# Kernel optimization log

Hardware: AMD Instinct MI355X
Metric: run time of the kernel (lower is better)

## Reference

```python
import jax, jax.numpy as jnp
import numpy as np

OUT_FEATURES = 4096
IN_FEATURES = 4096

# NF4 codebook (bitsandbytes normal-float 4-bit values)
_NF4_CODEBOOK = np.array([
    -1.0, -0.6961928, -0.52507305, -0.3949175, -0.28444138, -0.18477343,
    -0.09105004, 0.0, 0.0795803, 0.1609302, 0.2461123, 0.33791524,
    0.44070983, 0.562617, 0.72295684, 1.0], dtype=np.float32)


def setup_inputs() -> dict:
    key = jax.random.key(0)
    k_x, k_codes, k_scale, k_bias = jax.random.split(key, 4)
    x = jax.random.normal(k_x, (4, 2048, IN_FEATURES), dtype=jnp.float32)
    # packed uint8 nibble codes stored as int32 in [0, 256)
    packed_codes = jax.random.randint(
        k_codes, (OUT_FEATURES * IN_FEATURES // 2,), 0, 256, dtype=jnp.int32)
    # positive per-channel scales [out, 1]
    scale = jax.random.uniform(k_scale, (OUT_FEATURES, 1), dtype=jnp.float32) * 0.05 + 0.01
    bias = jax.random.normal(k_bias, (OUT_FEATURES,), dtype=jnp.float32)
    return {"x": x, "packed_codes": packed_codes, "scale": scale, "bias": bias}


def _dequantize_nf4(packed_codes, scale):
    codebook = jnp.asarray(_NF4_CODEBOOK)
    low = packed_codes & 15           # even positions
    high = (packed_codes >> 4) & 15   # odd positions
    # interleave: unpacked[0::2]=low, unpacked[1::2]=high
    idx = jnp.stack([low, high], axis=-1).reshape(-1)  # [out*in]
    w = codebook[idx].reshape(OUT_FEATURES, IN_FEATURES) * scale  # [out, in]
    return w


def reference(x, packed_codes, scale, bias):
    w = _dequantize_nf4(packed_codes, scale)
    # F.linear: x @ w.T + bias
    return jnp.einsum("bsi,oi->bso", x, w) + bias
```

## Files before the change

kernel.cpp:

```cpp
#include <hip/hip_runtime.h>
#include <stdint.h>

#define IN_F 4096
#define OUT_F 4096
#define M_ROWS 8192

__device__ __constant__ int c_nf4_i8[16] = {
    -127, -88, -67, -50, -36, -23, -12, 0, 10, 20, 31, 43, 56, 71, 92, 127};

typedef int i32x4 __attribute__((ext_vector_type(4)));

__global__ __launch_bounds__(256) void k_quant_x(
    const float* __restrict__ x, signed char* __restrict__ xq,
    float* __restrict__ steps) {
  const int row = blockIdx.x;
  const int tid = threadIdx.x;
  const float4* xr = (const float4*)(x + (size_t)row * IN_F);
  float4 v[4];
  float m = 0.0f;
#pragma unroll
  for (int i = 0; i < 4; ++i) {
    v[i] = xr[tid + 256 * i];
    m = fmaxf(m, fmaxf(fmaxf(fabsf(v[i].x), fabsf(v[i].y)),
                       fmaxf(fabsf(v[i].z), fabsf(v[i].w))));
  }
#pragma unroll
  for (int off = 32; off > 0; off >>= 1) m = fmaxf(m, __shfl_xor(m, off));
  __shared__ float wmax[4];
  if ((tid & 63) == 0) wmax[tid >> 6] = m;
  __syncthreads();
  m = fmaxf(fmaxf(wmax[0], wmax[1]), fmaxf(wmax[2], wmax[3]));
  const float inv = (m > 0.0f) ? 127.0f / m : 0.0f;
  if (tid == 0) steps[row] = m * (1.0f / 127.0f);
  int* oq = (int*)(xq + (size_t)row * IN_F);
#pragma unroll
  for (int i = 0; i < 4; ++i) {
    int q0 = (int)rintf(v[i].x * inv);
    int q1 = (int)rintf(v[i].y * inv);
    int q2 = (int)rintf(v[i].z * inv);
    int q3 = (int)rintf(v[i].w * inv);
    oq[tid + 256 * i] =
        (q0 & 255) | ((q1 & 255) << 8) | ((q2 & 255) << 16) | (q3 << 24);
  }
}

__global__ __launch_bounds__(256) void k_dequant(
    const int* __restrict__ packed, signed char* __restrict__ W) {
  __shared__ short lut[256];
  {
    const int b = threadIdx.x;
    const int lo = c_nf4_i8[b & 15], hi = c_nf4_i8[b >> 4];
    lut[b] = (short)((lo & 0xFF) | ((hi & 0xFF) << 8));
  }
  __syncthreads();
  const int tid = blockIdx.x * 256 + threadIdx.x;
  const int4 ca = ((const int4*)packed)[2 * tid];
  const int4 cb = ((const int4*)packed)[2 * tid + 1];
  union { short h[8]; int4 v; } o;
  o.h[0] = lut[ca.x]; o.h[1] = lut[ca.y]; o.h[2] = lut[ca.z]; o.h[3] = lut[ca.w];
  o.h[4] = lut[cb.x]; o.h[5] = lut[cb.y]; o.h[6] = lut[cb.z]; o.h[7] = lut[cb.w];
  ((int4*)W)[tid] = o.v;
}

#define GLL(gptr, lptr)                                          \
  __builtin_amdgcn_global_load_lds(                              \
      (__attribute__((address_space(1))) void*)(gptr),           \
      (__attribute__((address_space(3))) void*)(lptr), 16, 0, 0)

__global__ __launch_bounds__(256) void k_gemm(
    const signed char* __restrict__ A,
    const signed char* __restrict__ B,
    const float* __restrict__ steps,
    const float* __restrict__ scale,
    const float* __restrict__ bias,
    float* __restrict__ C) {
  __shared__ __align__(16) signed char sA[128 * 64];
  __shared__ __align__(16) signed char sB[128 * 64];
  const int tid = threadIdx.x;
  const int lane = tid & 63;
  const int w  = tid >> 6;
  const int wm = w >> 1;
  const int wn = w & 1;
  const int bm = blockIdx.y * 128;
  const int bn = blockIdx.x * 128;

  i32x4 acc[4][4] = {};

  const signed char* gA =
      A + (size_t)(bm + w * 32 + (lane >> 2)) * IN_F + (lane & 3) * 16;
  const signed char* gB =
      B + (size_t)(bn + w * 32 + (lane >> 2)) * IN_F + (lane & 3) * 16;
  signed char* lA = sA + w * 32 * 64;
  signed char* lB = sB + w * 32 * 64;

  const int fr = lane & 15;
  const int fk = (lane >> 4) * 16;

  for (int k0 = 0; k0 < IN_F; k0 += 64) {
    GLL(gA + k0, lA);
    GLL(gA + k0 + 16 * IN_F, lA + 16 * 64);
    GLL(gB + k0, lB);
    GLL(gB + k0 + 16 * IN_F, lB + 16 * 64);
    __syncthreads();

    i32x4 af[4], bf[4];
#pragma unroll
    for (int t = 0; t < 4; ++t) {
      af[t] = *(const i32x4*)&sA[(wm * 64 + t * 16 + fr) * 64 + fk];
      bf[t] = *(const i32x4*)&sB[(wn * 64 + t * 16 + fr) * 64 + fk];
    }
#pragma unroll
    for (int i = 0; i < 4; ++i)
#pragma unroll
      for (int j = 0; j < 4; ++j)
        acc[i][j] = __builtin_amdgcn_mfma_i32_16x16x64_i8(af[i], bf[j],
                                                          acc[i][j], 0, 0, 0);
    __syncthreads();
  }

  const int col0 = bn + wn * 64 + fr;
  const int row0 = bm + wm * 64 + (lane >> 4) * 4;
  float srow[4][4];
#pragma unroll
  for (int i = 0; i < 4; ++i)
#pragma unroll
    for (int r = 0; r < 4; ++r) srow[i][r] = steps[row0 + i * 16 + r];
#pragma unroll
  for (int j = 0; j < 4; ++j) {
    const int col = col0 + j * 16;
    const float fc = scale[col] * (1.0f / 127.0f);
    const float bv = bias[col];
#pragma unroll
    for (int i = 0; i < 4; ++i) {
      const int row = row0 + i * 16;
#pragma unroll
      for (int r = 0; r < 4; ++r)
        C[(size_t)(row + r) * OUT_F + col] =
            (float)acc[i][j][r] * (srow[i][r] * fc) + bv;
    }
  }
}

extern "C" void kernel_launch(void* const* d_in, const int* in_sizes, int n_in,
                              void* d_out, int out_size, void* d_ws, size_t ws_size,
                              hipStream_t stream) {
  const float* x      = (const float*)d_in[0];
  const int* packed   = (const int*)d_in[1];
  const float* scale  = (const float*)d_in[2];
  const float* bias   = (const float*)d_in[3];
  float* out = (float*)d_out;

  signed char* Xq = (signed char*)d_ws;
  signed char* Wq = Xq + (size_t)M_ROWS * IN_F;
  float* steps = (float*)(Wq + (size_t)OUT_F * IN_F);

  k_quant_x<<<M_ROWS, 256, 0, stream>>>(x, Xq, steps);
  k_dequant<<<(OUT_F * IN_F / 2) / (256 * 8), 256, 0, stream>>>(packed, Wq);
  dim3 grid(OUT_F / 128, M_ROWS / 128);
  k_gemm<<<grid, 256, 0, stream>>>(Xq, Wq, steps, scale, bias, out);
}
```

Measured before the change: 415.3 us.

## Switch int8 GEMM to 32x32x32 MFMA with K=128 tiles and XOR-swizzled LDS

Replaces the 16x16x64 int8 MFMA tiling with 32x32x32 MFMA instructions, giving each wave a 2x2 grid of 32x32 accumulators. The K step per shared-memory stage doubles to 128, which halves the number of barrier pairs over the K loop. The LDS layout uses an XOR swizzle on 16-byte chunks to avoid bank conflicts on the wider rows. Shared memory per block doubles to 32KB, which may reduce occupancy, and the epilogue now reads steps per element instead of caching them.

```diff
diff --git a/kernel.cpp b/kernel.cpp
--- a/kernel.cpp
+++ b/kernel.cpp
@@ -9,6 +9,7 @@
     -127, -88, -67, -50, -36, -23, -12, 0, 10, 20, 31, 43, 56, 71, 92, 127};
 
 typedef int i32x4 __attribute__((ext_vector_type(4)));
+typedef int i32x16 __attribute__((ext_vector_type(16)));
 
 __global__ __launch_bounds__(256) void k_quant_x(
     const float* __restrict__ x, signed char* __restrict__ xq,
@@ -74,8 +75,8 @@
     const float* __restrict__ scale,
     const float* __restrict__ bias,
     float* __restrict__ C) {
-  __shared__ __align__(16) signed char sA[128 * 64];
-  __shared__ __align__(16) signed char sB[128 * 64];
+  __shared__ __align__(16) signed char sA[128 * 128];
+  __shared__ __align__(16) signed char sB[128 * 128];
   const int tid = threadIdx.x;
   const int lane = tid & 63;
   const int w  = tid >> 6;
@@ -84,59 +85,57 @@
   const int bm = blockIdx.y * 128;
   const int bn = blockIdx.x * 128;
 
-  i32x4 acc[4][4] = {};
+  i32x16 acc[2][2] = {};
 
-  const signed char* gA =
-      A + (size_t)(bm + w * 32 + (lane >> 2)) * IN_F + (lane & 3) * 16;
-  const signed char* gB =
-      B + (size_t)(bn + w * 32 + (lane >> 2)) * IN_F + (lane & 3) * 16;
-  signed char* lA = sA + w * 32 * 64;
-  signed char* lB = sB + w * 32 * 64;
+  const int srow  = w * 32 + (lane >> 3);
+  const int schnk = (lane & 7) ^ (lane >> 3);
+  const signed char* gA = A + (size_t)(bm + srow) * IN_F + schnk * 16;
+  const signed char* gB = B + (size_t)(bn + srow) * IN_F + schnk * 16;
+  signed char* lA = sA + w * 32 * 128;
+  signed char* lB = sB + w * 32 * 128;
 
-  const int fr = lane & 15;
-  const int fk = (lane >> 4) * 16;
+  const int r31   = lane & 31;
+  const int khalf = lane >> 5;
+  const int rx7   = lane & 7;
 
-  for (int k0 = 0; k0 < IN_F; k0 += 64) {
-    GLL(gA + k0, lA);
-    GLL(gA + k0 + 16 * IN_F, lA + 16 * 64);
-    GLL(gB + k0, lB);
-    GLL(gB + k0 + 16 * IN_F, lB + 16 * 64);
+  for (int k0 = 0; k0 < IN_F; k0 += 128) {
+#pragma unroll
+    for (int g = 0; g < 4; ++g) {
+      GLL(gA + k0 + g * 8 * IN_F, lA + g * 1024);
+      GLL(gB + k0 + g * 8 * IN_F, lB + g * 1024);
+    }
     __syncthreads();
-
-    i32x4 af[4], bf[4];
 #pragma unroll
-    for (int t = 0; t < 4; ++t) {
-      af[t] = *(const i32x4*)&sA[(wm * 64 + t * 16 + fr) * 64 + fk];
-      bf[t] = *(const i32x4*)&sB[(wn * 64 + t * 16 + fr) * 64 + fk];
+    for (int ks = 0; ks < 4; ++ks) {
+      const int ch = ((2 * ks + khalf) ^ rx7) * 16;
+      i32x4 a0 = *(const i32x4*)&sA[(wm * 64      + r31) * 128 + ch];
+      i32x4 a1 = *(const i32x4*)&sA[(wm * 64 + 32 + r31) * 128 + ch];
+      i32x4 b0 = *(const i32x4*)&sB[(wn * 64      + r31) * 128 + ch];
+      i32x4 b1 = *(const i32x4*)&sB[(wn * 64 + 32 + r31) * 128 + ch];
+      acc[0][0] = __builtin_amdgcn_mfma_i32_32x32x32_i8(a0, b0, acc[0][0], 0, 0, 0);
+      acc[0][1] = __builtin_amdgcn_mfma_i32_32x32x32_i8(a0, b1, acc[0][1], 0, 0, 0);
+      acc[1][0] = __builtin_amdgcn_mfma_i32_32x32x32_i8(a1, b0, acc[1][0], 0, 0, 0);
+      acc[1][1] = __builtin_amdgcn_mfma_i32_32x32x32_i8(a1, b1, acc[1][1], 0, 0, 0);
     }
-#pragma unroll
-    for (int i = 0; i < 4; ++i)
-#pragma unroll
-      for (int j = 0; j < 4; ++j)
-        acc[i][j] = __builtin_amdgcn_mfma_i32_16x16x64_i8(af[i], bf[j],
-                                                          acc[i][j], 0, 0, 0);
     __syncthreads();
   }
 
-  const int col0 = bn + wn * 64 + fr;
-  const int row0 = bm + wm * 64 + (lane >> 4) * 4;
-  float srow[4][4];
+  const int colb = bn + wn * 64 + r31;
+  const int rowb = bm + wm * 64 + 4 * khalf;
 #pragma unroll
-  for (int i = 0; i < 4; ++i)
-#pragma unroll
-    for (int r = 0; r < 4; ++r) srow[i][r] = steps[row0 + i * 16 + r];
-#pragma unroll
-  for (int j = 0; j < 4; ++j) {
-    const int col = col0 + j * 16;
+  for (int fj = 0; fj < 2; ++fj) {
+    const int col = colb + fj * 32;
     const float fc = scale[col] * (1.0f / 127.0f);
     const float bv = bias[col];
 #pragma unroll
-    for (int i = 0; i < 4; ++i) {
-      const int row = row0 + i * 16;
+    for (int fi = 0; fi < 2; ++fi) {
+      const int row0 = rowb + fi * 32;
 #pragma unroll
-      for (int r = 0; r < 4; ++r)
-        C[(size_t)(row + r) * OUT_F + col] =
-            (float)acc[i][j][r] * (srow[i][r] * fc) + bv;
+      for (int reg = 0; reg < 16; ++reg) {
+        const int row = row0 + (reg & 3) + 8 * (reg >> 2);
+        C[(size_t)row * OUT_F + col] =
+            (float)acc[fi][fj][reg] * (steps[row] * fc) + bv;
+      }
     }
   }
 }
```

New measurement: 393.2 us. 5.3% less time.
